# Optimization experiments

Measured on AMD Instinct MI355X. Metric: run time of the kernel, lower is better.

The kernel has to match this reference:

```python
import jax, jax.numpy as jnp
import numpy as np


def setup_inputs() -> dict:
    key = jax.random.key(0)
    k1, k2, k3, k4 = jax.random.split(key, 4)
    z = jax.random.normal(k1, (16, 4096, 512), dtype=jnp.float32)
    codebook = jax.random.normal(k2, (1024, 256), dtype=jnp.float32)
    w_down = jax.random.normal(k3, (256, 512), dtype=jnp.float32) * 0.04
    w_up = jax.random.normal(k4, (512, 256), dtype=jnp.float32) * 0.06
    return {"z": z, "codebook": codebook, "w_down": w_down, "w_up": w_up}


def reference(z, codebook, w_down, w_up):
    b, t, _ = z.shape
    # proj_down: nn.Linear(512 -> 256, no bias): x @ W^T
    z_e = jnp.einsum('btd,ed->bte', z, w_down)  # [b, t, 256]
    z_flat = z_e.reshape(b * t, -1)
    # squared euclidean distances to codebook entries
    dist = (jnp.sum(z_flat ** 2, axis=1, keepdims=True)
            - 2.0 * z_flat @ codebook.T
            + jnp.sum(codebook ** 2, axis=1)[None, :])  # [bt, n]
    code = jnp.argmin(dist, axis=1).reshape(b, t)  # [b, t] int
    z_q = codebook[code]  # [b, t, 256]
    # per-batch mean losses (detach semantics irrelevant for fwd values)
    commitment_loss = jnp.mean((z_q - z_e) ** 2, axis=(1, 2))  # [b]
    codebook_loss = jnp.mean((z_q - z_e) ** 2, axis=(1, 2))  # [b]
    # straight-through estimator (training mode)
    z_q_ste = z_e + jax.lax.stop_gradient(z_q - z_e)
    # proj_up: nn.Linear(256 -> 512, no bias)
    z_out = jnp.einsum('bte,de->btd', z_q_ste, w_up)  # [b, t, 512]
    return z_out, commitment_loss, codebook_loss, code
```

## Files before the change

### kernel.cpp

```cpp
#include <hip/hip_runtime.h>

#define TOKS    65536
#define D_IN    512
#define D_E     256
#define NCODES  1024

#define FLAG_CAP 16384
#define TAU      0.05f

using s16x8 = __attribute__((ext_vector_type(8))) short;
using f32x4 = __attribute__((ext_vector_type(4))) float;

__device__ __forceinline__ unsigned short bf16_rne(float x) {
    unsigned u = __float_as_uint(x);
    u += 0x7fffu + ((u >> 16) & 1u);
    return (unsigned short)(u >> 16);
}
__device__ __forceinline__ float bf16_to_f(unsigned short h) {
    return __uint_as_float(((unsigned)h) << 16);
}

__device__ __forceinline__ void unpack_il(uint4 u0, uint4 u1, s16x8& hi, s16x8& lo) {
    union { unsigned u[4]; s16x8 v; } H, L;
    H.u[0] = (u0.y & 0xffff0000u) | (u0.x >> 16);
    H.u[1] = (u0.w & 0xffff0000u) | (u0.z >> 16);
    H.u[2] = (u1.y & 0xffff0000u) | (u1.x >> 16);
    H.u[3] = (u1.w & 0xffff0000u) | (u1.z >> 16);
    L.u[0] = (u0.y << 16) | (u0.x & 0xffffu);
    L.u[1] = (u0.w << 16) | (u0.z & 0xffffu);
    L.u[2] = (u1.y << 16) | (u1.x & 0xffffu);
    L.u[3] = (u1.w << 16) | (u1.z & 0xffffu);
    hi = H.v; lo = L.v;
}

__global__ __launch_bounds__(256) void rownorm_kernel(
        const float* __restrict__ src, float* __restrict__ dst) {
    int row  = blockIdx.x * 4 + (threadIdx.x >> 6);
    int lane = threadIdx.x & 63;
    float4 v = *(const float4*)(src + (long)row * 256 + lane * 4);
    float s = v.x * v.x + v.y * v.y + v.z * v.z + v.w * v.w;
    #pragma unroll
    for (int off = 32; off; off >>= 1) s += __shfl_xor(s, off, 64);
    if (lane == 0) dst[row] = s;
}

__global__ __launch_bounds__(256) void split_kernel(
        const float* __restrict__ src, unsigned short* __restrict__ hi,
        unsigned short* __restrict__ lo, int n) {
    int i = blockIdx.x * 256 + threadIdx.x;
    if (i < n) {
        float x = src[i];
        unsigned short hb = bf16_rne(x);
        hi[i] = hb;
        lo[i] = bf16_rne(x - bf16_to_f(hb));
    }
}

__global__ __launch_bounds__(256) void cb_up_kernel(
        const float* __restrict__ cb, const float* __restrict__ w_up,
        float* __restrict__ cb_up) {
    __shared__ float cbs4[4][256];
    const int tid = threadIdx.x;
    const int r0  = blockIdx.x * 4;
    #pragma unroll
    for (int r = 0; r < 4; ++r) cbs4[r][tid] = cb[(long)(r0 + r) * 256 + tid];
    __syncthreads();
    float acc[4][2] = {};
    const float* wa = w_up + (long)tid * 256;
    const float* wb = w_up + (long)(tid + 256) * 256;
    #pragma unroll 4
    for (int k = 0; k < 256; k += 4) {
        float4 a = *(const float4*)(wa + k);
        float4 b = *(const float4*)(wb + k);
        #pragma unroll
        for (int r = 0; r < 4; ++r) {
            float4 c = *(const float4*)&cbs4[r][k];
            acc[r][0] += a.x * c.x + a.y * c.y + a.z * c.z + a.w * c.w;
            acc[r][1] += b.x * c.x + b.y * c.y + b.z * c.z + b.w * c.w;
        }
    }
    #pragma unroll
    for (int r = 0; r < 4; ++r) {
        cb_up[(long)(r0 + r) * 512 + tid]       = acc[r][0];
        cb_up[(long)(r0 + r) * 512 + tid + 256] = acc[r][1];
    }
}

__global__ __launch_bounds__(256) void gather_kernel(
        const float4* __restrict__ cb_up4, const int* __restrict__ code_i,
        float4* __restrict__ out4) {
    const int base = blockIdx.x * 1024 + threadIdx.x;
    #pragma unroll
    for (int j = 0; j < 4; ++j) {
        int g   = base + j * 256;
        int tok = g >> 7;
        int col = g & 127;
        out4[g] = cb_up4[(long)code_i[tok] * 128 + col];
    }
}

__global__ __launch_bounds__(256, 2) void gemm_down_mfma_kernel(
        const float* __restrict__ z, const unsigned short* __restrict__ wd_hi,
        const unsigned short* __restrict__ wd_lo, unsigned* __restrict__ ze_il,
        float* __restrict__ znorm) {
    __shared__ __align__(16) unsigned short wds[2][2][256][32];

    const int tid  = threadIdx.x;
    const int w    = tid >> 6;
    const int lane = tid & 63;
    const int lr   = lane & 15;
    const int lg   = lane >> 4;
    const int t0   = blockIdx.x * 128 + w * 32;

    f32x4 acc[2][16] = {};

    auto stage = [&](int b, int ks) {
        #pragma unroll
        for (int i = 0; i < 8; ++i) {
            const int j = i * 256 + tid;
            const int p = j >> 10, rw = (j >> 2) & 255, sub = j & 3;
            const s16x8 v = *(const s16x8*)((p ? wd_lo : wd_hi)
                                            + (long)rw * 512 + ks * 32 + sub * 8);
            *(s16x8*)((unsigned short*)wds[b] + j * 8) = v;
        }
    };

    stage(0, 0);

    #pragma unroll 1
    for (int ks = 0; ks < 16; ++ks) {
        const int b = ks & 1;
        __syncthreads();
        if (ks < 15) stage(b ^ 1, ks + 1);

        s16x8 ah[2], al[2];
        #pragma unroll
        for (int tt = 0; tt < 2; ++tt) {
            const float* zp = z + (long)(t0 + tt * 16 + lr) * 512 + ks * 32 + lg * 8;
            float4 x0 = *(const float4*)zp;
            float4 x1 = *(const float4*)(zp + 4);
            float xs[8] = {x0.x, x0.y, x0.z, x0.w, x1.x, x1.y, x1.z, x1.w};
            #pragma unroll
            for (int j = 0; j < 8; ++j) {
                unsigned hb = __float_as_uint(xs[j]) & 0xffff0000u;
                float rem = xs[j] - __uint_as_float(hb);
                ah[tt][j] = (short)(hb >> 16);
                al[tt][j] = (short)bf16_rne(rem);
            }
        }

        #pragma unroll
        for (int nt = 0; nt < 16; ++nt) {
            const s16x8 bh = *(const s16x8*)&wds[b][0][nt * 16 + lr][lg * 8];
            const s16x8 bl = *(const s16x8*)&wds[b][1][nt * 16 + lr][lg * 8];
            #pragma unroll
            for (int tt = 0; tt < 2; ++tt) {
                acc[tt][nt] = __builtin_amdgcn_mfma_f32_16x16x32_bf16(al[tt], bh, acc[tt][nt], 0, 0, 0);
                acc[tt][nt] = __builtin_amdgcn_mfma_f32_16x16x32_bf16(ah[tt], bl, acc[tt][nt], 0, 0, 0);
                acc[tt][nt] = __builtin_amdgcn_mfma_f32_16x16x32_bf16(ah[tt], bh, acc[tt][nt], 0, 0, 0);
            }
        }
    }

    #pragma unroll
    for (int tt = 0; tt < 2; ++tt) {
        float ns[4] = {0.f, 0.f, 0.f, 0.f};
        #pragma unroll
        for (int nt = 0; nt < 16; ++nt)
            #pragma unroll
            for (int r = 0; r < 4; ++r) {
                float x = acc[tt][nt][r];
                ns[r] += x * x;
                unsigned short hb = bf16_rne(x);
                unsigned short lb = bf16_rne(x - bf16_to_f(hb));
                ze_il[(long)(t0 + tt * 16 + lg * 4 + r) * 256 + nt * 16 + lr] =
                    ((unsigned)hb << 16) | lb;
            }
        #pragma unroll
        for (int r = 0; r < 4; ++r) {
            float s = ns[r];
            s += __shfl_xor(s, 1, 64);
            s += __shfl_xor(s, 2, 64);
            s += __shfl_xor(s, 4, 64);
            s += __shfl_xor(s, 8, 64);
            if (lr == 0) znorm[t0 + tt * 16 + lg * 4 + r] = s;
        }
    }
}

__global__ __launch_bounds__(256, 2) void argmin_mfma_kernel(
        const unsigned* __restrict__ ze_il,
        const unsigned short* __restrict__ cb_hi, const unsigned short* __restrict__ cb_lo,
        const float* __restrict__ cnorm, const float* __restrict__ znorm,
        int* __restrict__ code_i, float* __restrict__ code_f,
        float* __restrict__ loss_acc, int* __restrict__ flag_cnt,
        int4* __restrict__ flag_list) {
    __shared__ __align__(16) unsigned short cbs[2][64][136];

    const int tid  = threadIdx.x;
    const int w    = tid >> 6;
    const int lane = tid & 63;
    const int lr   = lane & 15;
    const int lg   = lane >> 4;
    const int t0   = blockIdx.x * 128;

    s16x8 ah[2][8], al[2][8];
    {
        const int tokA = t0 + w * 32 + lr;
        #pragma unroll
        for (int tt = 0; tt < 2; ++tt) {
            const unsigned* pz = ze_il + (long)(tokA + tt * 16) * 256 + lg * 8;
            #pragma unroll
            for (int ks = 0; ks < 8; ++ks) {
                uint4 u0 = *(const uint4*)(pz + ks * 32);
                uint4 u1 = *(const uint4*)(pz + ks * 32 + 4);
                unpack_il(u0, u1, ah[tt][ks], al[tt][ks]);
            }
        }
    }

    const int lane_base = lr * 136 + lg * 8;

    float d1[8], d2[8];
    int   i1[8], i2[8];
    #pragma unroll
    for (int s = 0; s < 8; ++s) { d1[s] = 3.4e38f; d2[s] = 3.4e38f; i1[s] = 0; i2[s] = 0; }

    #pragma unroll 1
    for (int c = 0; c < 16; ++c) {
        const int c0 = c * 64;
        f32x4 acc[2][4] = {};

        #pragma unroll
        for (int kc = 0; kc < 2; ++kc) {
            __syncthreads();
            {
                const int r = tid & 63, q = tid >> 6;
                const unsigned short* src = (q & 2 ? cb_lo : cb_hi)
                                            + (c0 + r) * 256 + kc * 128 + (q & 1) * 64;
                unsigned short* dst = &cbs[q >> 1][r][0] + (q & 1) * 64;
                #pragma unroll
                for (int i = 0; i < 8; ++i)
                    *(s16x8*)(dst + i * 8) = *(const s16x8*)(src + i * 8);
            }
            __syncthreads();

            #pragma unroll
            for (int k4 = 0; k4 < 4; ++k4) {
                const int ks = kc * 4 + k4;
                #pragma unroll
                for (int nt = 0; nt < 4; ++nt) {
                    const int off = lane_base + nt * 2176 + k4 * 32;
                    const s16x8 bh = *(const s16x8*)(&cbs[0][0][0] + off);
                    const s16x8 bl = *(const s16x8*)(&cbs[1][0][0] + off);
                    #pragma unroll
                    for (int tt = 0; tt < 2; ++tt) {
                        acc[tt][nt] = __builtin_amdgcn_mfma_f32_16x16x32_bf16(al[tt][ks], bh, acc[tt][nt], 0, 0, 0);
                        acc[tt][nt] = __builtin_amdgcn_mfma_f32_16x16x32_bf16(ah[tt][ks], bl, acc[tt][nt], 0, 0, 0);
                        acc[tt][nt] = __builtin_amdgcn_mfma_f32_16x16x32_bf16(ah[tt][ks], bh, acc[tt][nt], 0, 0, 0);
                    }
                }
            }
        }

        #pragma unroll
        for (int nt = 0; nt < 4; ++nt) {
            const int idx = c0 + nt * 16 + lr;
            const float cn = cnorm[idx];
            #pragma unroll
            for (int tt = 0; tt < 2; ++tt)
                #pragma unroll
                for (int r = 0; r < 4; ++r) {
                    float d = cn - 2.0f * acc[tt][nt][r];
                    const int s = tt * 4 + r;
                    if (d < d1[s])      { d2[s] = d1[s]; i2[s] = i1[s]; d1[s] = d; i1[s] = idx; }
                    else if (d < d2[s]) { d2[s] = d;     i2[s] = idx; }
                }
        }
    }

    #pragma unroll
    for (int off = 1; off <= 8; off <<= 1) {
        #pragma unroll
        for (int s = 0; s < 8; ++s) {
            float od1 = __shfl_xor(d1[s], off, 64);
            int   oi1 = __shfl_xor(i1[s], off, 64);
            float od2 = __shfl_xor(d2[s], off, 64);
            int   oi2 = __shfl_xor(i2[s], off, 64);
            bool take = (od1 < d1[s]) || (od1 == d1[s] && oi1 < i1[s]);
            float w1 = take ? od1 : d1[s];  int wi1 = take ? oi1 : i1[s];
            float l1 = take ? d1[s] : od1;  int li1 = take ? i1[s] : oi1;
            float w2 = take ? od2 : d2[s];  int wi2 = take ? oi2 : i2[s];
            bool t2 = (l1 < w2) || (l1 == w2 && li1 < wi2);
            d1[s] = w1; i1[s] = wi1;
            d2[s] = t2 ? l1 : w2;
            i2[s] = t2 ? li1 : wi2;
        }
    }

    if (lr == 0) {
        float lsum = 0.0f;
        #pragma unroll
        for (int s = 0; s < 8; ++s) {
            const int tok = t0 + w * 32 + (s >> 2) * 16 + lg * 4 + (s & 3);
            code_i[tok] = i1[s];
            code_f[tok] = (float)i1[s];
            const float rec = d1[s] + znorm[tok];
            lsum += rec;
            if (d2[s] - d1[s] < TAU) {
                int slot = atomicAdd(flag_cnt, 1);
                if (slot < FLAG_CAP)
                    flag_list[slot] = make_int4(tok, i1[s], i2[s], __float_as_int(rec));
            }
        }
        atomicAdd(loss_acc + (t0 >> 12), lsum);
    }
}

__global__ __launch_bounds__(256) void refine_kernel(
        const float* __restrict__ z, const float* __restrict__ w_down,
        const float* __restrict__ cb, const int* __restrict__ flag_cnt,
        const int4* __restrict__ flag_list, int* __restrict__ code_i,
        float* __restrict__ code_f, float* __restrict__ loss_acc) {
    __shared__ float zrow[512];
    __shared__ float redA[4], redB[4];
    const int tid = threadIdx.x;
    int n = *flag_cnt;
    if (n > FLAG_CAP) n = FLAG_CAP;

    for (int it = blockIdx.x; it < n; it += gridDim.x) {
        const int4 f = flag_list[it];
        const int tok = f.x, ia = f.y, ib = f.z;
        __syncthreads();
        zrow[tid]       = z[(long)tok * 512 + tid];
        zrow[tid + 256] = z[(long)tok * 512 + 256 + tid];
        __syncthreads();

        float s = 0.0f;
        const float* wr = w_down + (long)tid * 512;
        #pragma unroll 4
        for (int k = 0; k < 512; k += 4) {
            float4 a = *(const float4*)(wr + k);
            s += a.x * zrow[k] + a.y * zrow[k + 1] + a.z * zrow[k + 2] + a.w * zrow[k + 3];
        }
        float da = s - cb[(long)ia * 256 + tid]; da *= da;
        float db = s - cb[(long)ib * 256 + tid]; db *= db;
        #pragma unroll
        for (int off = 32; off; off >>= 1) {
            da += __shfl_xor(da, off, 64);
            db += __shfl_xor(db, off, 64);
        }
        if ((tid & 63) == 0) { redA[tid >> 6] = da; redB[tid >> 6] = db; }
        __syncthreads();
        if (tid == 0) {
            float ea = redA[0] + redA[1] + redA[2] + redA[3];
            float eb = redB[0] + redB[1] + redB[2] + redB[3];
            float ebest = ea; int ibest = ia;
            if (eb < ea || (eb == ea && ib < ia)) { ebest = eb; ibest = ib; }
            if (ibest != ia) { code_i[tok] = ibest; code_f[tok] = (float)ibest; }
            atomicAdd(loss_acc + (tok >> 12), ebest - __int_as_float(f.w));
        }
    }
}

__global__ void finalize_kernel(const float* __restrict__ loss_acc,
                                float* __restrict__ out_losses) {
    int i = threadIdx.x;
    if (i < 16) {
        float v = loss_acc[i] * (1.0f / 1048576.0f);
        out_losses[i]      = v;
        out_losses[16 + i] = v;
    }
}

extern "C" void kernel_launch(void* const* d_in, const int* in_sizes, int n_in,
                              void* d_out, int out_size, void* d_ws, size_t ws_size,
                              hipStream_t stream) {
    const float* z      = (const float*)d_in[0];
    const float* cb     = (const float*)d_in[1];
    const float* w_down = (const float*)d_in[2];
    const float* w_up   = (const float*)d_in[3];

    float* out        = (float*)d_out;
    float* z_out      = out;
    float* out_losses = out + 33554432;
    float* code_f     = out + 33554464;

    unsigned* ze_il = (unsigned*)d_out;

    char* ws = (char*)d_ws;
    unsigned short* cb_hi = (unsigned short*)(ws);
    unsigned short* cb_lo = (unsigned short*)(ws + 524288);
    unsigned short* wd_hi = (unsigned short*)(ws + 1048576);
    unsigned short* wd_lo = (unsigned short*)(ws + 1310720);
    int*   code_i    = (int*)  (ws + 1572864);
    float* cnorm     = (float*)(ws + 1835008);
    float* znorm     = (float*)(ws + 1839104);
    int4*  flag_list = (int4*) (ws + 2101248);
    float* cb_up     = (float*)(ws + 2363392);
    float* loss_acc  = (float*)(ws + 4460544);
    int*   flag_cnt  = (int*)  (ws + 4460608);

    hipMemsetAsync(ws + 4460544, 0, 128, stream);

    rownorm_kernel<<<NCODES / 4, 256, 0, stream>>>(cb, cnorm);

    split_kernel<<<1024, 256, 0, stream>>>(cb, cb_hi, cb_lo, NCODES * D_E);
    split_kernel<<<512, 256, 0, stream>>>(w_down, wd_hi, wd_lo, D_E * D_IN);

    cb_up_kernel<<<NCODES / 4, 256, 0, stream>>>(cb, w_up, cb_up);

    gemm_down_mfma_kernel<<<TOKS / 128, 256, 0, stream>>>(
        z, wd_hi, wd_lo, ze_il, znorm);

    argmin_mfma_kernel<<<TOKS / 128, 256, 0, stream>>>(
        ze_il, cb_hi, cb_lo, cnorm, znorm, code_i, code_f, loss_acc,
        flag_cnt, flag_list);

    refine_kernel<<<256, 256, 0, stream>>>(z, w_down, cb, flag_cnt, flag_list,
                                           code_i, code_f, loss_acc);

    gather_kernel<<<TOKS * 512 / 4 / 1024, 256, 0, stream>>>(
        (const float4*)cb_up, code_i, (float4*)z_out);

    finalize_kernel<<<1, 64, 0, stream>>>(loss_acc, out_losses);
}
```

Measured before the change: 505.9 us.

## Halve per-block token tile in GEMM and argmin kernels for higher occupancy

Both the down-projection GEMM and the argmin kernel now process 64 tokens per block (16 per wave) instead of 128, with launch bounds raised to 4 blocks per SM. The GEMM also drops double-buffering of the weight slices in LDS, using a single buffer with two barriers per k-step. The aim is to cut register and LDS pressure so more waves can hide memory latency. In exchange, each weight and codebook tile loaded into LDS is reused by half as many tokens, which doubles that load traffic, and the GEMM loses its load/compute overlap.

```diff
diff --git a/kernel.cpp b/kernel.cpp
--- a/kernel.cpp
+++ b/kernel.cpp
@@ -99,44 +99,38 @@
     }
 }
 
-__global__ __launch_bounds__(256, 2) void gemm_down_mfma_kernel(
+__global__ __launch_bounds__(256, 4) void gemm_down_mfma_kernel(
         const float* __restrict__ z, const unsigned short* __restrict__ wd_hi,
         const unsigned short* __restrict__ wd_lo, unsigned* __restrict__ ze_il,
         float* __restrict__ znorm) {
-    __shared__ __align__(16) unsigned short wds[2][2][256][32];
+    __shared__ __align__(16) unsigned short wds[2][256][32];
 
     const int tid  = threadIdx.x;
     const int w    = tid >> 6;
     const int lane = tid & 63;
     const int lr   = lane & 15;
     const int lg   = lane >> 4;
-    const int t0   = blockIdx.x * 128 + w * 32;
-
-    f32x4 acc[2][16] = {};
-
-    auto stage = [&](int b, int ks) {
-        #pragma unroll
-        for (int i = 0; i < 8; ++i) {
-            const int j = i * 256 + tid;
-            const int p = j >> 10, rw = (j >> 2) & 255, sub = j & 3;
-            const s16x8 v = *(const s16x8*)((p ? wd_lo : wd_hi)
-                                            + (long)rw * 512 + ks * 32 + sub * 8);
-            *(s16x8*)((unsigned short*)wds[b] + j * 8) = v;
-        }
-    };
-
-    stage(0, 0);
+    const int t0   = blockIdx.x * 64 + w * 16;
+
+    f32x4 acc[16] = {};
 
     #pragma unroll 1
     for (int ks = 0; ks < 16; ++ks) {
-        const int b = ks & 1;
         __syncthreads();
-        if (ks < 15) stage(b ^ 1, ks + 1);
-
-        s16x8 ah[2], al[2];
-        #pragma unroll
-        for (int tt = 0; tt < 2; ++tt) {
-            const float* zp = z + (long)(t0 + tt * 16 + lr) * 512 + ks * 32 + lg * 8;
+        {
+            #pragma unroll
+            for (int i = 0; i < 8; ++i) {
+                const int j = i * 256 + tid;
+                const int p = j >> 10, rw = (j >> 2) & 255, sub = j & 3;
+                const s16x8 v = *(const s16x8*)((p ? wd_lo : wd_hi)
+                                                + (long)rw * 512 + ks * 32 + sub * 8);
+                *(s16x8*)((unsigned short*)wds + j * 8) = v;
+            }
+        }
+
+        s16x8 ah, al;
+        {
+            const float* zp = z + (long)(t0 + lr) * 512 + ks * 32 + lg * 8;
             float4 x0 = *(const float4*)zp;
             float4 x1 = *(const float4*)(zp + 4);
             float xs[8] = {x0.x, x0.y, x0.z, x0.w, x1.x, x1.y, x1.z, x1.w};
@@ -144,51 +138,46 @@
             for (int j = 0; j < 8; ++j) {
                 unsigned hb = __float_as_uint(xs[j]) & 0xffff0000u;
                 float rem = xs[j] - __uint_as_float(hb);
-                ah[tt][j] = (short)(hb >> 16);
-                al[tt][j] = (short)bf16_rne(rem);
-            }
-        }
+                ah[j] = (short)(hb >> 16);
+                al[j] = (short)bf16_rne(rem);
+            }
+        }
+        __syncthreads();
 
         #pragma unroll
         for (int nt = 0; nt < 16; ++nt) {
-            const s16x8 bh = *(const s16x8*)&wds[b][0][nt * 16 + lr][lg * 8];
-            const s16x8 bl = *(const s16x8*)&wds[b][1][nt * 16 + lr][lg * 8];
-            #pragma unroll
-            for (int tt = 0; tt < 2; ++tt) {
-                acc[tt][nt] = __builtin_amdgcn_mfma_f32_16x16x32_bf16(al[tt], bh, acc[tt][nt], 0, 0, 0);
-                acc[tt][nt] = __builtin_amdgcn_mfma_f32_16x16x32_bf16(ah[tt], bl, acc[tt][nt], 0, 0, 0);
-                acc[tt][nt] = __builtin_amdgcn_mfma_f32_16x16x32_bf16(ah[tt], bh, acc[tt][nt], 0, 0, 0);
-            }
-        }
-    }
-
-    #pragma unroll
-    for (int tt = 0; tt < 2; ++tt) {
-        float ns[4] = {0.f, 0.f, 0.f, 0.f};
-        #pragma unroll
-        for (int nt = 0; nt < 16; ++nt)
-            #pragma unroll
-            for (int r = 0; r < 4; ++r) {
-                float x = acc[tt][nt][r];
-                ns[r] += x * x;
-                unsigned short hb = bf16_rne(x);
-                unsigned short lb = bf16_rne(x - bf16_to_f(hb));
-                ze_il[(long)(t0 + tt * 16 + lg * 4 + r) * 256 + nt * 16 + lr] =
-                    ((unsigned)hb << 16) | lb;
-            }
+            const s16x8 bh = *(const s16x8*)&wds[0][nt * 16 + lr][lg * 8];
+            const s16x8 bl = *(const s16x8*)&wds[1][nt * 16 + lr][lg * 8];
+            acc[nt] = __builtin_amdgcn_mfma_f32_16x16x32_bf16(al, bh, acc[nt], 0, 0, 0);
+            acc[nt] = __builtin_amdgcn_mfma_f32_16x16x32_bf16(ah, bl, acc[nt], 0, 0, 0);
+            acc[nt] = __builtin_amdgcn_mfma_f32_16x16x32_bf16(ah, bh, acc[nt], 0, 0, 0);
+        }
+    }
+
+    float ns[4] = {0.f, 0.f, 0.f, 0.f};
+    #pragma unroll
+    for (int nt = 0; nt < 16; ++nt)
         #pragma unroll
         for (int r = 0; r < 4; ++r) {
-            float s = ns[r];
-            s += __shfl_xor(s, 1, 64);
-            s += __shfl_xor(s, 2, 64);
-            s += __shfl_xor(s, 4, 64);
-            s += __shfl_xor(s, 8, 64);
-            if (lr == 0) znorm[t0 + tt * 16 + lg * 4 + r] = s;
-        }
-    }
-}
-
-__global__ __launch_bounds__(256, 2) void argmin_mfma_kernel(
+            float x = acc[nt][r];
+            ns[r] += x * x;
+            unsigned short hb = bf16_rne(x);
+            unsigned short lb = bf16_rne(x - bf16_to_f(hb));
+            ze_il[(long)(t0 + lg * 4 + r) * 256 + nt * 16 + lr] =
+                ((unsigned)hb << 16) | lb;
+        }
+    #pragma unroll
+    for (int r = 0; r < 4; ++r) {
+        float s = ns[r];
+        s += __shfl_xor(s, 1, 64);
+        s += __shfl_xor(s, 2, 64);
+        s += __shfl_xor(s, 4, 64);
+        s += __shfl_xor(s, 8, 64);
+        if (lr == 0) znorm[t0 + lg * 4 + r] = s;
+    }
+}
+
+__global__ __launch_bounds__(256, 4) void argmin_mfma_kernel(
         const unsigned* __restrict__ ze_il,
         const unsigned short* __restrict__ cb_hi, const unsigned short* __restrict__ cb_lo,
         const float* __restrict__ cnorm, const float* __restrict__ znorm,
@@ -202,34 +191,30 @@
     const int lane = tid & 63;
     const int lr   = lane & 15;
     const int lg   = lane >> 4;
-    const int t0   = blockIdx.x * 128;
-
-    s16x8 ah[2][8], al[2][8];
+    const int t0   = blockIdx.x * 64;
+
+    s16x8 ah[8], al[8];
     {
-        const int tokA = t0 + w * 32 + lr;
-        #pragma unroll
-        for (int tt = 0; tt < 2; ++tt) {
-            const unsigned* pz = ze_il + (long)(tokA + tt * 16) * 256 + lg * 8;
-            #pragma unroll
-            for (int ks = 0; ks < 8; ++ks) {
-                uint4 u0 = *(const uint4*)(pz + ks * 32);
-                uint4 u1 = *(const uint4*)(pz + ks * 32 + 4);
-                unpack_il(u0, u1, ah[tt][ks], al[tt][ks]);
-            }
+        const unsigned* pz = ze_il + (long)(t0 + w * 16 + lr) * 256 + lg * 8;
+        #pragma unroll
+        for (int ks = 0; ks < 8; ++ks) {
+            uint4 u0 = *(const uint4*)(pz + ks * 32);
+            uint4 u1 = *(const uint4*)(pz + ks * 32 + 4);
+            unpack_il(u0, u1, ah[ks], al[ks]);
         }
     }
 
     const int lane_base = lr * 136 + lg * 8;
 
-    float d1[8], d2[8];
-    int   i1[8], i2[8];
-    #pragma unroll
-    for (int s = 0; s < 8; ++s) { d1[s] = 3.4e38f; d2[s] = 3.4e38f; i1[s] = 0; i2[s] = 0; }
+    float d1[4], d2[4];
+    int   i1[4], i2[4];
+    #pragma unroll
+    for (int s = 0; s < 4; ++s) { d1[s] = 3.4e38f; d2[s] = 3.4e38f; i1[s] = 0; i2[s] = 0; }
 
     #pragma unroll 1
     for (int c = 0; c < 16; ++c) {
         const int c0 = c * 64;
-        f32x4 acc[2][4] = {};
+        f32x4 acc[4] = {};
 
         #pragma unroll
         for (int kc = 0; kc < 2; ++kc) {
@@ -253,12 +238,9 @@
                     const int off = lane_base + nt * 2176 + k4 * 32;
                     const s16x8 bh = *(const s16x8*)(&cbs[0][0][0] + off);
                     const s16x8 bl = *(const s16x8*)(&cbs[1][0][0] + off);
-                    #pragma unroll
-                    for (int tt = 0; tt < 2; ++tt) {
-                        acc[tt][nt] = __builtin_amdgcn_mfma_f32_16x16x32_bf16(al[tt][ks], bh, acc[tt][nt], 0, 0, 0);
-                        acc[tt][nt] = __builtin_amdgcn_mfma_f32_16x16x32_bf16(ah[tt][ks], bl, acc[tt][nt], 0, 0, 0);
-                        acc[tt][nt] = __builtin_amdgcn_mfma_f32_16x16x32_bf16(ah[tt][ks], bh, acc[tt][nt], 0, 0, 0);
-                    }
+                    acc[nt] = __builtin_amdgcn_mfma_f32_16x16x32_bf16(al[ks], bh, acc[nt], 0, 0, 0);
+                    acc[nt] = __builtin_amdgcn_mfma_f32_16x16x32_bf16(ah[ks], bl, acc[nt], 0, 0, 0);
+                    acc[nt] = __builtin_amdgcn_mfma_f32_16x16x32_bf16(ah[ks], bh, acc[nt], 0, 0, 0);
                 }
             }
         }
@@ -268,21 +250,18 @@
             const int idx = c0 + nt * 16 + lr;
             const float cn = cnorm[idx];
             #pragma unroll
-            for (int tt = 0; tt < 2; ++tt)
-                #pragma unroll
-                for (int r = 0; r < 4; ++r) {
-                    float d = cn - 2.0f * acc[tt][nt][r];
-                    const int s = tt * 4 + r;
-                    if (d < d1[s])      { d2[s] = d1[s]; i2[s] = i1[s]; d1[s] = d; i1[s] = idx; }
-                    else if (d < d2[s]) { d2[s] = d;     i2[s] = idx; }
-                }
+            for (int r = 0; r < 4; ++r) {
+                float d = cn - 2.0f * acc[nt][r];
+                if (d < d1[r])      { d2[r] = d1[r]; i2[r] = i1[r]; d1[r] = d; i1[r] = idx; }
+                else if (d < d2[r]) { d2[r] = d;     i2[r] = idx; }
+            }
         }
     }
 
     #pragma unroll
     for (int off = 1; off <= 8; off <<= 1) {
         #pragma unroll
-        for (int s = 0; s < 8; ++s) {
+        for (int s = 0; s < 4; ++s) {
             float od1 = __shfl_xor(d1[s], off, 64);
             int   oi1 = __shfl_xor(i1[s], off, 64);
             float od2 = __shfl_xor(d2[s], off, 64);
@@ -301,8 +280,8 @@
     if (lr == 0) {
         float lsum = 0.0f;
         #pragma unroll
-        for (int s = 0; s < 8; ++s) {
-            const int tok = t0 + w * 32 + (s >> 2) * 16 + lg * 4 + (s & 3);
+        for (int s = 0; s < 4; ++s) {
+            const int tok = t0 + w * 16 + lg * 4 + s;
             code_i[tok] = i1[s];
             code_f[tok] = (float)i1[s];
             const float rec = d1[s] + znorm[tok];
@@ -410,10 +389,10 @@
 
     cb_up_kernel<<<NCODES / 4, 256, 0, stream>>>(cb, w_up, cb_up);
 
-    gemm_down_mfma_kernel<<<TOKS / 128, 256, 0, stream>>>(
+    gemm_down_mfma_kernel<<<TOKS / 64, 256, 0, stream>>>(
         z, wd_hi, wd_lo, ze_il, znorm);
 
-    argmin_mfma_kernel<<<TOKS / 128, 256, 0, stream>>>(
+    argmin_mfma_kernel<<<TOKS / 64, 256, 0, stream>>>(
         ze_il, cb_hi, cb_lo, cnorm, znorm, code_i, code_f, loss_acc,
         flag_cnt, flag_list);
 
```

New measurement: 627.4 us. +24.0%, slower.
